# Kernel optimization log

Measured on AMD Instinct MI355X. Metric: run time of the kernel, lower is better.

The kernel has to match this reference:

```python
import jax, jax.numpy as jnp
import numpy as np

T, B, DIN, DLAT = 512, 128, 256, 512

def setup_inputs() -> dict:
    key = jax.random.key(0)
    k1, k2, k3, k4, k5 = jax.random.split(key, 5)
    s_i = 1.0 / np.sqrt(DIN)
    s_h = 1.0 / np.sqrt(DLAT)
    return {
        "X": jax.random.normal(k1, (T, B, DIN), dtype=jnp.float32),
        "h": jnp.zeros((B, DLAT), dtype=jnp.float32),
        "Wi": jax.random.uniform(k2, (DLAT, DIN), jnp.float32, -s_i, s_i),
        "bi": jax.random.uniform(k3, (DLAT,), jnp.float32, -s_i, s_i),
        "Wh": jax.random.uniform(k4, (DLAT, DLAT), jnp.float32, -s_h, s_h),
        "bh": jax.random.uniform(k5, (DLAT,), jnp.float32, -s_h, s_h),
    }

def reference(X, h, Wi, bi, Wh, bh):
    # Precompute input projection for all timesteps at once: [T,B,DLAT]
    Xi = jnp.einsum('tbd,ld->tbl', X, Wi) + bi + bh
    def step(h_prev, xi_t):
        h_t = jnp.tanh(xi_t + h_prev @ Wh.T)  # [B, DLAT]
        return h_t, h_t
    _, H = jax.lax.scan(step, h, Xi)
    return H  # [T, B, DLAT]
```

## Files before the change

kernel.cpp:

```cpp
#include <hip/hip_runtime.h>

#define T_STEPS 512
#define BATCH   128
#define DIN     256
#define DLAT    512

typedef __bf16 bf16x8 __attribute__((ext_vector_type(8)));
typedef float  f32x4  __attribute__((ext_vector_type(4)));
typedef int    i32x4  __attribute__((ext_vector_type(4)));
typedef unsigned long long u64;

__device__ __forceinline__ unsigned int f2bf2(float a, float b) {
  unsigned int ua = __float_as_uint(a);
  unsigned int ub = __float_as_uint(b);
  ua = (ua + 0x7FFFu + ((ua >> 16) & 1u)) >> 16;
  ub = (ub + 0x7FFFu + ((ub >> 16) & 1u)) >> 16;
  return ua | (ub << 16);
}

__device__ __forceinline__ uint4 pack8(float4 f0, float4 f1) {
  uint4 r;
  r.x = f2bf2(f0.x, f0.y);
  r.y = f2bf2(f0.z, f0.w);
  r.z = f2bf2(f1.x, f1.y);
  r.w = f2bf2(f1.z, f1.w);
  return r;
}

extern "C" __global__ __launch_bounds__(256) void pk_wh(
    const float* __restrict__ Wh, unsigned int* __restrict__ out) {
  int idx = blockIdx.x * 256 + threadIdx.x;
  const float* src = Wh + (long)idx * 8;
  float4 f0 = *(const float4*)src;
  float4 f1 = *(const float4*)(src + 4);
  uint4 v = pack8(f0, f1);
  *(uint4*)(out + (long)idx * 4) = v;
}

extern "C" __global__ __launch_bounds__(256) void xi_gemm(
    const float* __restrict__ X, const float* __restrict__ Wi,
    const float* __restrict__ bi, const float* __restrict__ bh,
    float* __restrict__ XiOut) {
  extern __shared__ char smem[];
  char*  sX    = smem;
  char*  sW    = smem + 65536;
  float* sBias = (float*)(smem + 131072);

  const int tid = threadIdx.x;
  const long m0 = (long)blockIdx.x * 128;
  const int  n0 = blockIdx.y * 128;

  #pragma unroll
  for (int c = 0; c < 16; ++c) {
    int id = c * 256 + tid;
    int r  = id >> 5;
    int kc = (id & 31) << 3;
    const float* sx = X + (m0 + r) * DIN + kc;
    float4 a0 = *(const float4*)sx;
    float4 a1 = *(const float4*)(sx + 4);
    int ax = ((r << 9) + (kc << 1)) ^ ((r & 7) << 4);
    *(uint4*)(sX + ax) = pack8(a0, a1);
    const float* sw = Wi + (n0 + r) * DIN + kc;
    float4 b0 = *(const float4*)sw;
    float4 b1 = *(const float4*)(sw + 4);
    *(uint4*)(sW + ax) = pack8(b0, b1);
  }
  if (tid < 128) sBias[tid] = bi[n0 + tid] + bh[n0 + tid];
  __syncthreads();

  const int w = tid >> 6, lane = tid & 63;
  const int wm = (w >> 1) * 64, wn = (w & 1) * 64;
  const int lm = lane & 15, lq = lane >> 4;

  f32x4 acc[4][4];
  #pragma unroll
  for (int nt = 0; nt < 4; ++nt) {
    float bv = sBias[wn + nt * 16 + lm];
    #pragma unroll
    for (int mt = 0; mt < 4; ++mt) acc[mt][nt] = f32x4{bv, bv, bv, bv};
  }

  #pragma unroll
  for (int k0 = 0; k0 < 8; ++k0) {
    int kb = (k0 << 6) + (lq << 4);
    bf16x8 af[4], bfr[4];
    #pragma unroll
    for (int mt = 0; mt < 4; ++mt) {
      int row = wm + mt * 16 + lm;
      int ax = ((row << 9) + kb) ^ ((row & 7) << 4);
      af[mt] = __builtin_bit_cast(bf16x8, *(uint4*)(sX + ax));
    }
    #pragma unroll
    for (int nt = 0; nt < 4; ++nt) {
      int row = wn + nt * 16 + lm;
      int ax = ((row << 9) + kb) ^ ((row & 7) << 4);
      bfr[nt] = __builtin_bit_cast(bf16x8, *(uint4*)(sW + ax));
    }
    #pragma unroll
    for (int mt = 0; mt < 4; ++mt)
      #pragma unroll
      for (int nt = 0; nt < 4; ++nt)
        acc[mt][nt] = __builtin_amdgcn_mfma_f32_16x16x32_bf16(af[mt], bfr[nt], acc[mt][nt], 0, 0, 0);
  }

  #pragma unroll
  for (int mt = 0; mt < 4; ++mt) {
    #pragma unroll
    for (int e = 0; e < 4; ++e) {
      long m = m0 + wm + mt * 16 + (lq << 2) + e;
      float* dst = XiOut + m * DLAT + n0 + wn + lm;
      #pragma unroll
      for (int nt = 0; nt < 4; ++nt)
        dst[nt * 16] = acc[mt][nt][e];
    }
  }
}

extern "C" __global__ __launch_bounds__(512, 2) void rnn_scan(
    const float* __restrict__ h0, const unsigned short* __restrict__ WhP,
    float* __restrict__ HO, u64* __restrict__ hx,
    unsigned int* __restrict__ flags) {
  __shared__ uint4 sH4[1024];
  char* sH = (char*)sH4;

  const int tid = threadIdx.x;
  const int w = tid >> 6, lane = tid & 63;
  const int lm = lane & 15, lq = lane >> 4;
  const int g  = blockIdx.x & 7;
  const int q  = blockIdx.x >> 3;
  const int r0 = g << 4;
  const int nt = (q << 7) + (w << 4);

  i32x4 wreg[16];
  {
    const unsigned short* base = WhP + (nt + lm) * DLAT + (lq << 3);
    #pragma unroll
    for (int kq = 0; kq < 16; ++kq)
      wreg[kq] = *(const i32x4*)(base + kq * 32);
    #pragma unroll
    for (int kq = 0; kq < 16; ++kq)
      asm("" : "+v"(wreg[kq]));
  }

  #pragma unroll
  for (int c = 0; c < 2; ++c) {
    int id = c * 512 + tid;
    int m = id >> 6, kc = (id & 63) << 3;
    const float* src = h0 + (r0 + m) * DLAT + kc;
    float4 f0 = *(const float4*)src;
    float4 f1 = *(const float4*)(src + 4);
    int ax = ((m << 10) + (kc << 1)) ^ ((m & 7) << 4);
    *(uint4*)(sH + ax) = pack8(f0, f1);
  }
  __syncthreads();

  const int mask  = (lm & 7) << 4;
  const int hbase = (lm << 10) + (lq << 4);
  const int ncol  = nt + (lq << 2);
  unsigned int* fgrp = flags + (g << 11);
  const int sq = (q + 1 + lane) & 3;

  float4 xi = *(const float4*)(HO + (long)(r0 + lm) * DLAT + ncol);

  for (int t = 0; t < T_STEPS; ++t) {
    f32x4 a0 = f32x4{0.f, 0.f, 0.f, 0.f};
    f32x4 a1 = f32x4{0.f, 0.f, 0.f, 0.f};
    f32x4 a2 = f32x4{0.f, 0.f, 0.f, 0.f};
    f32x4 a3 = f32x4{0.f, 0.f, 0.f, 0.f};
    #pragma unroll
    for (int kq = 0; kq < 16; kq += 4) {
      bf16x8 hb0 = __builtin_bit_cast(bf16x8, *(uint4*)(sH + ((hbase + kq * 64) ^ mask)));
      bf16x8 hb1 = __builtin_bit_cast(bf16x8, *(uint4*)(sH + ((hbase + (kq + 1) * 64) ^ mask)));
      bf16x8 hb2 = __builtin_bit_cast(bf16x8, *(uint4*)(sH + ((hbase + (kq + 2) * 64) ^ mask)));
      bf16x8 hb3 = __builtin_bit_cast(bf16x8, *(uint4*)(sH + ((hbase + (kq + 3) * 64) ^ mask)));
      a0 = __builtin_amdgcn_mfma_f32_16x16x32_bf16(
          __builtin_bit_cast(bf16x8, wreg[kq]), hb0, a0, 0, 0, 0);
      a1 = __builtin_amdgcn_mfma_f32_16x16x32_bf16(
          __builtin_bit_cast(bf16x8, wreg[kq + 1]), hb1, a1, 0, 0, 0);
      a2 = __builtin_amdgcn_mfma_f32_16x16x32_bf16(
          __builtin_bit_cast(bf16x8, wreg[kq + 2]), hb2, a2, 0, 0, 0);
      a3 = __builtin_amdgcn_mfma_f32_16x16x32_bf16(
          __builtin_bit_cast(bf16x8, wreg[kq + 3]), hb3, a3, 0, 0, 0);
    }

    float hv[4];
    #pragma unroll
    for (int e = 0; e < 4; ++e) {
      float z = (a0[e] + a1[e]) + (a2[e] + a3[e]) + ((float*)&xi)[e];
      float ex = __expf(2.0f * z);
      hv[e] = 1.0f - 2.0f / (ex + 1.0f);
    }

    if (t + 1 < T_STEPS) {
      u64* hxg = hx + ((long)(t & 1) << 14) + ((long)g << 11);
      u64 v = ((u64)f2bf2(hv[2], hv[3]) << 32) | (u64)f2bf2(hv[0], hv[1]);

      __hip_atomic_store(&hxg[(lm << 7) + (ncol >> 2)], v,
                         __ATOMIC_RELAXED, __HIP_MEMORY_SCOPE_AGENT);
      asm volatile("s_waitcnt vmcnt(0)" ::: "memory");
      __syncthreads();

      if (tid == 0)
        __hip_atomic_store(&fgrp[(q << 9) + t], 1u,
                           __ATOMIC_RELAXED, __HIP_MEMORY_SCOPE_AGENT);

      {
        int ax = ((lm << 10) + (ncol << 1)) ^ mask;
        *(u64*)(sH + ax) = v;
        float4 o; o.x = hv[0]; o.y = hv[1]; o.z = hv[2]; o.w = hv[3];
        *(float4*)(HO + ((long)t * BATCH + r0 + lm) * DLAT + ncol) = o;
        xi = *(const float4*)(HO + ((long)(t + 1) * BATCH + r0 + lm) * DLAT + ncol);
      }

      for (;;) {
        unsigned int fv = (lane < 3)
            ? __hip_atomic_load(&fgrp[(sq << 9) + t], __ATOMIC_RELAXED, __HIP_MEMORY_SCOPE_AGENT)
            : 1u;
        if (!__any(fv == 0u)) break;
        __builtin_amdgcn_s_sleep(1);
      }
      asm volatile("" ::: "memory");

      {
        int m = tid >> 5, j = tid & 31;
        #pragma unroll
        for (int s = 1; s < 4; ++s) {
          int qq = (q + s) & 3;
          int idx = (m << 7) + (qq << 5) + j;
          u64 hvv = __hip_atomic_load(&hxg[idx],
                                      __ATOMIC_RELAXED, __HIP_MEMORY_SCOPE_AGENT);
          int ax = ((m << 10) + (((qq << 5) + j) << 3)) ^ ((m & 7) << 4);
          *(u64*)(sH + ax) = hvv;
        }
      }

      __syncthreads();
    } else {
      float4 o; o.x = hv[0]; o.y = hv[1]; o.z = hv[2]; o.w = hv[3];
      *(float4*)(HO + ((long)t * BATCH + r0 + lm) * DLAT + ncol) = o;
    }
  }
}

extern "C" void kernel_launch(void* const* d_in, const int* in_sizes, int n_in,
                              void* d_out, int out_size, void* d_ws, size_t ws_size,
                              hipStream_t stream) {
  const float* X  = (const float*)d_in[0];
  const float* h0 = (const float*)d_in[1];
  const float* Wi = (const float*)d_in[2];
  const float* bi = (const float*)d_in[3];
  const float* Wh = (const float*)d_in[4];
  const float* bh = (const float*)d_in[5];
  float* out = (float*)d_out;

  unsigned int* whp   = (unsigned int*)d_ws;
  u64*          hx    = (u64*)((char*)d_ws + 524288);
  unsigned int* flags = (unsigned int*)((char*)d_ws + 786432);

  hipMemsetAsync(flags, 0, 65536, stream);

  hipFuncSetAttribute((const void*)xi_gemm, hipFuncAttributeMaxDynamicSharedMemorySize, 131584);

  pk_wh<<<128, 256, 0, stream>>>(Wh, whp);
  xi_gemm<<<dim3(512, 4), 256, 131584, stream>>>(X, Wi, bi, bh, out);
  rnn_scan<<<32, 512, 0, stream>>>(h0, (const unsigned short*)whp, out, hx, flags);
}
```

Before: 1.306 ms.

## Load recurrent h fragments directly from global exchange buffer, drop LDS staging

The scan kernel no longer copies the exchanged hidden state into shared memory each step. Each lane now reads its MFMA B-operand fragments straight from the double-buffered global exchange array. A new pk_h0 kernel seeds buffer 0 with the bf16-packed initial state. This removes the per-step LDS write, the LDS re-read and one block-wide barrier from the serial critical path. In exchange, every wave issues 32 global loads per step and re-reads the full 16x512 state, so L2 traffic rises sharply and L2 latency moves onto the MFMA input path.

```diff
diff --git a/kernel.cpp b/kernel.cpp
--- a/kernel.cpp
+++ b/kernel.cpp
@@ -9,6 +9,7 @@
 typedef float  f32x4  __attribute__((ext_vector_type(4)));
 typedef int    i32x4  __attribute__((ext_vector_type(4)));
 typedef unsigned long long u64;
+typedef unsigned long long u64x2 __attribute__((ext_vector_type(2)));
 
 __device__ __forceinline__ unsigned int f2bf2(float a, float b) {
   unsigned int ua = __float_as_uint(a);
@@ -35,6 +36,16 @@
   float4 f1 = *(const float4*)(src + 4);
   uint4 v = pack8(f0, f1);
   *(uint4*)(out + (long)idx * 4) = v;
+}
+
+extern "C" __global__ __launch_bounds__(256) void pk_h0(
+    const float* __restrict__ h0, u64* __restrict__ hx) {
+  int idx = blockIdx.x * 256 + threadIdx.x;
+  int r = idx >> 7, j = idx & 127;
+  int g = r >> 4, m = r & 15;
+  float4 f = *(const float4*)(h0 + (long)r * DLAT + j * 4);
+  u64 v = ((u64)f2bf2(f.z, f.w) << 32) | (u64)f2bf2(f.x, f.y);
+  hx[((long)g << 11) + (m << 7) + j] = v;
 }
 
 extern "C" __global__ __launch_bounds__(256) void xi_gemm(
@@ -117,12 +128,8 @@
 }
 
 extern "C" __global__ __launch_bounds__(512, 2) void rnn_scan(
-    const float* __restrict__ h0, const unsigned short* __restrict__ WhP,
-    float* __restrict__ HO, u64* __restrict__ hx,
-    unsigned int* __restrict__ flags) {
-  __shared__ uint4 sH4[1024];
-  char* sH = (char*)sH4;
-
+    const unsigned short* __restrict__ WhP, float* __restrict__ HO,
+    u64* __restrict__ hx, unsigned int* __restrict__ flags) {
   const int tid = threadIdx.x;
   const int w = tid >> 6, lane = tid & 63;
   const int lm = lane & 15, lq = lane >> 4;
@@ -142,45 +149,43 @@
       asm("" : "+v"(wreg[kq]));
   }
 
-  #pragma unroll
-  for (int c = 0; c < 2; ++c) {
-    int id = c * 512 + tid;
-    int m = id >> 6, kc = (id & 63) << 3;
-    const float* src = h0 + (r0 + m) * DLAT + kc;
-    float4 f0 = *(const float4*)src;
-    float4 f1 = *(const float4*)(src + 4);
-    int ax = ((m << 10) + (kc << 1)) ^ ((m & 7) << 4);
-    *(uint4*)(sH + ax) = pack8(f0, f1);
-  }
-  __syncthreads();
-
-  const int mask  = (lm & 7) << 4;
-  const int hbase = (lm << 10) + (lq << 4);
-  const int ncol  = nt + (lq << 2);
+  const int ncol = nt + (lq << 2);
   unsigned int* fgrp = flags + (g << 11);
   const int sq = (q + 1 + lane) & 3;
+  u64* hgrp = hx + ((long)g << 11);
+  const int fb  = (lm << 7) + (lq << 1);
+  const int pub = (lm << 7) + (ncol >> 2);
 
   float4 xi = *(const float4*)(HO + (long)(r0 + lm) * DLAT + ncol);
 
   for (int t = 0; t < T_STEPS; ++t) {
+    const u64* hs = hgrp + ((long)(t & 1) << 14);
+
+    u64 fA[16], fB[16];
+    #pragma unroll
+    for (int kq = 0; kq < 16; ++kq) {
+      fA[kq] = __hip_atomic_load(&hs[fb + kq * 8],     __ATOMIC_RELAXED, __HIP_MEMORY_SCOPE_AGENT);
+      fB[kq] = __hip_atomic_load(&hs[fb + kq * 8 + 1], __ATOMIC_RELAXED, __HIP_MEMORY_SCOPE_AGENT);
+    }
+
     f32x4 a0 = f32x4{0.f, 0.f, 0.f, 0.f};
     f32x4 a1 = f32x4{0.f, 0.f, 0.f, 0.f};
     f32x4 a2 = f32x4{0.f, 0.f, 0.f, 0.f};
     f32x4 a3 = f32x4{0.f, 0.f, 0.f, 0.f};
     #pragma unroll
     for (int kq = 0; kq < 16; kq += 4) {
-      bf16x8 hb0 = __builtin_bit_cast(bf16x8, *(uint4*)(sH + ((hbase + kq * 64) ^ mask)));
-      bf16x8 hb1 = __builtin_bit_cast(bf16x8, *(uint4*)(sH + ((hbase + (kq + 1) * 64) ^ mask)));
-      bf16x8 hb2 = __builtin_bit_cast(bf16x8, *(uint4*)(sH + ((hbase + (kq + 2) * 64) ^ mask)));
-      bf16x8 hb3 = __builtin_bit_cast(bf16x8, *(uint4*)(sH + ((hbase + (kq + 3) * 64) ^ mask)));
+      u64x2 p0 = u64x2{fA[kq],     fB[kq]};
+      u64x2 p1 = u64x2{fA[kq + 1], fB[kq + 1]};
+      u64x2 p2 = u64x2{fA[kq + 2], fB[kq + 2]};
+      u64x2 p3 = u64x2{fA[kq + 3], fB[kq + 3]};
       a0 = __builtin_amdgcn_mfma_f32_16x16x32_bf16(
-          __builtin_bit_cast(bf16x8, wreg[kq]), hb0, a0, 0, 0, 0);
+          __builtin_bit_cast(bf16x8, wreg[kq]),     __builtin_bit_cast(bf16x8, p0), a0, 0, 0, 0);
       a1 = __builtin_amdgcn_mfma_f32_16x16x32_bf16(
-          __builtin_bit_cast(bf16x8, wreg[kq + 1]), hb1, a1, 0, 0, 0);
+          __builtin_bit_cast(bf16x8, wreg[kq + 1]), __builtin_bit_cast(bf16x8, p1), a1, 0, 0, 0);
       a2 = __builtin_amdgcn_mfma_f32_16x16x32_bf16(
-          __builtin_bit_cast(bf16x8, wreg[kq + 2]), hb2, a2, 0, 0, 0);
+          __builtin_bit_cast(bf16x8, wreg[kq + 2]), __builtin_bit_cast(bf16x8, p2), a2, 0, 0, 0);
       a3 = __builtin_amdgcn_mfma_f32_16x16x32_bf16(
-          __builtin_bit_cast(bf16x8, wreg[kq + 3]), hb3, a3, 0, 0, 0);
+          __builtin_bit_cast(bf16x8, wreg[kq + 3]), __builtin_bit_cast(bf16x8, p3), a3, 0, 0, 0);
     }
 
     float hv[4];
@@ -192,10 +197,8 @@
     }
 
     if (t + 1 < T_STEPS) {
-      u64* hxg = hx + ((long)(t & 1) << 14) + ((long)g << 11);
       u64 v = ((u64)f2bf2(hv[2], hv[3]) << 32) | (u64)f2bf2(hv[0], hv[1]);
-
-      __hip_atomic_store(&hxg[(lm << 7) + (ncol >> 2)], v,
+      __hip_atomic_store(&hgrp[((long)((t + 1) & 1) << 14) + pub], v,
                          __ATOMIC_RELAXED, __HIP_MEMORY_SCOPE_AGENT);
       asm volatile("s_waitcnt vmcnt(0)" ::: "memory");
       __syncthreads();
@@ -205,8 +208,6 @@
                            __ATOMIC_RELAXED, __HIP_MEMORY_SCOPE_AGENT);
 
       {
-        int ax = ((lm << 10) + (ncol << 1)) ^ mask;
-        *(u64*)(sH + ax) = v;
         float4 o; o.x = hv[0]; o.y = hv[1]; o.z = hv[2]; o.w = hv[3];
         *(float4*)(HO + ((long)t * BATCH + r0 + lm) * DLAT + ncol) = o;
         xi = *(const float4*)(HO + ((long)(t + 1) * BATCH + r0 + lm) * DLAT + ncol);
@@ -220,21 +221,6 @@
         __builtin_amdgcn_s_sleep(1);
       }
       asm volatile("" ::: "memory");
-
-      {
-        int m = tid >> 5, j = tid & 31;
-        #pragma unroll
-        for (int s = 1; s < 4; ++s) {
-          int qq = (q + s) & 3;
-          int idx = (m << 7) + (qq << 5) + j;
-          u64 hvv = __hip_atomic_load(&hxg[idx],
-                                      __ATOMIC_RELAXED, __HIP_MEMORY_SCOPE_AGENT);
-          int ax = ((m << 10) + (((qq << 5) + j) << 3)) ^ ((m & 7) << 4);
-          *(u64*)(sH + ax) = hvv;
-        }
-      }
-
-      __syncthreads();
     } else {
       float4 o; o.x = hv[0]; o.y = hv[1]; o.z = hv[2]; o.w = hv[3];
       *(float4*)(HO + ((long)t * BATCH + r0 + lm) * DLAT + ncol) = o;
@@ -262,6 +248,7 @@
   hipFuncSetAttribute((const void*)xi_gemm, hipFuncAttributeMaxDynamicSharedMemorySize, 131584);
 
   pk_wh<<<128, 256, 0, stream>>>(Wh, whp);
+  pk_h0<<<64, 256, 0, stream>>>(h0, hx);
   xi_gemm<<<dim3(512, 4), 256, 131584, stream>>>(X, Wi, bi, bh, out);
-  rnn_scan<<<32, 512, 0, stream>>>(h0, (const unsigned short*)whp, out, hx, flags);
-}
+  rnn_scan<<<32, 512, 0, stream>>>((const unsigned short*)whp, out, hx, flags);
+}
```

New measurement: 4.325 ms. +231.0%, slower.

## Replace flag-based cross-block sync with tagged data words and double-buffered LDS

Applied to the files above, without the earlier changes.

Each published bf16 hidden value now carries the step index in its upper 16 bits, so consumer blocks poll the data itself instead of waiting for a separate flag store after a vmcnt wait and block barrier. This removes one __syncthreads, the store-to-flag round trip and the sleep in the spin loop. The shared-memory hidden state is double-buffered so the next step's buffer can be filled without a barrier before the MFMA reads of the current one. In exchange, the exchange traffic doubles because each bf16 value occupies 32 bits, and polling becomes more aggressive without s_sleep.

```diff
diff --git a/kernel.cpp b/kernel.cpp
--- a/kernel.cpp
+++ b/kernel.cpp
@@ -118,10 +118,9 @@
 
 extern "C" __global__ __launch_bounds__(512, 2) void rnn_scan(
     const float* __restrict__ h0, const unsigned short* __restrict__ WhP,
-    float* __restrict__ HO, u64* __restrict__ hx,
-    unsigned int* __restrict__ flags) {
-  __shared__ uint4 sH4[1024];
-  char* sH = (char*)sH4;
+    float* __restrict__ HO, u64* __restrict__ hx) {
+  __shared__ uint4 sHbuf[2048];
+  char* sB = (char*)sHbuf;
 
   const int tid = threadIdx.x;
   const int w = tid >> 6, lane = tid & 63;
@@ -150,29 +149,38 @@
     float4 f0 = *(const float4*)src;
     float4 f1 = *(const float4*)(src + 4);
     int ax = ((m << 10) + (kc << 1)) ^ ((m & 7) << 4);
-    *(uint4*)(sH + ax) = pack8(f0, f1);
+    *(uint4*)(sB + ax) = pack8(f0, f1);
   }
   __syncthreads();
 
   const int mask  = (lm & 7) << 4;
   const int hbase = (lm << 10) + (lq << 4);
   const int ncol  = nt + (lq << 2);
-  unsigned int* fgrp = flags + (g << 11);
-  const int sq = (q + 1 + lane) & 3;
+  u64* hgrp = hx + ((long)g << 12);
+  const int pubi = (lm << 8) + (ncol >> 1);
+  const int rm = tid >> 5, rj = tid & 31;
+  const int q1 = (q + 1) & 3, q2 = (q + 2) & 3, q3 = (q + 3) & 3;
+  const int i1 = (rm << 8) + (q1 << 6) + (rj << 1);
+  const int i2 = (rm << 8) + (q2 << 6) + (rj << 1);
+  const int i3 = (rm << 8) + (q3 << 6) + (rj << 1);
+  const u64 tagmask = 0xFFFF0000FFFF0000ull;
 
   float4 xi = *(const float4*)(HO + (long)(r0 + lm) * DLAT + ncol);
 
   for (int t = 0; t < T_STEPS; ++t) {
+    char* cur = sB + ((t & 1) << 14);
+    char* nxt = sB + (((t + 1) & 1) << 14);
+
     f32x4 a0 = f32x4{0.f, 0.f, 0.f, 0.f};
     f32x4 a1 = f32x4{0.f, 0.f, 0.f, 0.f};
     f32x4 a2 = f32x4{0.f, 0.f, 0.f, 0.f};
     f32x4 a3 = f32x4{0.f, 0.f, 0.f, 0.f};
     #pragma unroll
     for (int kq = 0; kq < 16; kq += 4) {
-      bf16x8 hb0 = __builtin_bit_cast(bf16x8, *(uint4*)(sH + ((hbase + kq * 64) ^ mask)));
-      bf16x8 hb1 = __builtin_bit_cast(bf16x8, *(uint4*)(sH + ((hbase + (kq + 1) * 64) ^ mask)));
-      bf16x8 hb2 = __builtin_bit_cast(bf16x8, *(uint4*)(sH + ((hbase + (kq + 2) * 64) ^ mask)));
-      bf16x8 hb3 = __builtin_bit_cast(bf16x8, *(uint4*)(sH + ((hbase + (kq + 3) * 64) ^ mask)));
+      bf16x8 hb0 = __builtin_bit_cast(bf16x8, *(uint4*)(cur + ((hbase + kq * 64) ^ mask)));
+      bf16x8 hb1 = __builtin_bit_cast(bf16x8, *(uint4*)(cur + ((hbase + (kq + 1) * 64) ^ mask)));
+      bf16x8 hb2 = __builtin_bit_cast(bf16x8, *(uint4*)(cur + ((hbase + (kq + 2) * 64) ^ mask)));
+      bf16x8 hb3 = __builtin_bit_cast(bf16x8, *(uint4*)(cur + ((hbase + (kq + 3) * 64) ^ mask)));
       a0 = __builtin_amdgcn_mfma_f32_16x16x32_bf16(
           __builtin_bit_cast(bf16x8, wreg[kq]), hb0, a0, 0, 0, 0);
       a1 = __builtin_amdgcn_mfma_f32_16x16x32_bf16(
@@ -191,47 +199,60 @@
       hv[e] = 1.0f - 2.0f / (ex + 1.0f);
     }
 
+    unsigned int pr01 = f2bf2(hv[0], hv[1]);
+    unsigned int pr23 = f2bf2(hv[2], hv[3]);
+
     if (t + 1 < T_STEPS) {
-      u64* hxg = hx + ((long)(t & 1) << 14) + ((long)g << 11);
-      u64 v = ((u64)f2bf2(hv[2], hv[3]) << 32) | (u64)f2bf2(hv[0], hv[1]);
-
-      __hip_atomic_store(&hxg[(lm << 7) + (ncol >> 2)], v,
-                         __ATOMIC_RELAXED, __HIP_MEMORY_SCOPE_AGENT);
-      asm volatile("s_waitcnt vmcnt(0)" ::: "memory");
-      __syncthreads();
-
-      if (tid == 0)
-        __hip_atomic_store(&fgrp[(q << 9) + t], 1u,
-                           __ATOMIC_RELAXED, __HIP_MEMORY_SCOPE_AGENT);
+      u64* ps = hgrp + ((long)((t + 1) & 1) << 15);
+      {
+        unsigned int tg = (unsigned int)(t + 1) << 16;
+        u64 p0 = (u64)(tg | (pr01 & 0xFFFFu)) | ((u64)(tg | (pr01 >> 16)) << 32);
+        u64 p1 = (u64)(tg | (pr23 & 0xFFFFu)) | ((u64)(tg | (pr23 >> 16)) << 32);
+        __hip_atomic_store(&ps[pubi],     p0, __ATOMIC_RELAXED, __HIP_MEMORY_SCOPE_AGENT);
+        __hip_atomic_store(&ps[pubi + 1], p1, __ATOMIC_RELAXED, __HIP_MEMORY_SCOPE_AGENT);
+      }
 
       {
         int ax = ((lm << 10) + (ncol << 1)) ^ mask;
-        *(u64*)(sH + ax) = v;
+        *(u64*)(nxt + ax) = (u64)pr01 | ((u64)pr23 << 32);
+      }
+      {
         float4 o; o.x = hv[0]; o.y = hv[1]; o.z = hv[2]; o.w = hv[3];
         *(float4*)(HO + ((long)t * BATCH + r0 + lm) * DLAT + ncol) = o;
         xi = *(const float4*)(HO + ((long)(t + 1) * BATCH + r0 + lm) * DLAT + ncol);
       }
 
-      for (;;) {
-        unsigned int fv = (lane < 3)
-            ? __hip_atomic_load(&fgrp[(sq << 9) + t], __ATOMIC_RELAXED, __HIP_MEMORY_SCOPE_AGENT)
-            : 1u;
-        if (!__any(fv == 0u)) break;
-        __builtin_amdgcn_s_sleep(1);
-      }
-      asm volatile("" ::: "memory");
-
-      {
-        int m = tid >> 5, j = tid & 31;
-        #pragma unroll
-        for (int s = 1; s < 4; ++s) {
-          int qq = (q + s) & 3;
-          int idx = (m << 7) + (qq << 5) + j;
-          u64 hvv = __hip_atomic_load(&hxg[idx],
-                                      __ATOMIC_RELAXED, __HIP_MEMORY_SCOPE_AGENT);
-          int ax = ((m << 10) + (((qq << 5) + j) << 3)) ^ ((m & 7) << 4);
-          *(u64*)(sH + ax) = hvv;
+      u64 d1a, d1b, d2a, d2b, d3a, d3b;
+      {
+        const u64 tagpat = ((u64)(unsigned int)(t + 1) << 48) |
+                           ((u64)(unsigned int)(t + 1) << 16);
+        for (;;) {
+          d1a = __hip_atomic_load(&ps[i1],     __ATOMIC_RELAXED, __HIP_MEMORY_SCOPE_AGENT);
+          d1b = __hip_atomic_load(&ps[i1 + 1], __ATOMIC_RELAXED, __HIP_MEMORY_SCOPE_AGENT);
+          d2a = __hip_atomic_load(&ps[i2],     __ATOMIC_RELAXED, __HIP_MEMORY_SCOPE_AGENT);
+          d2b = __hip_atomic_load(&ps[i2 + 1], __ATOMIC_RELAXED, __HIP_MEMORY_SCOPE_AGENT);
+          d3a = __hip_atomic_load(&ps[i3],     __ATOMIC_RELAXED, __HIP_MEMORY_SCOPE_AGENT);
+          d3b = __hip_atomic_load(&ps[i3 + 1], __ATOMIC_RELAXED, __HIP_MEMORY_SCOPE_AGENT);
+          bool ok = ((d1a & tagmask) == tagpat) & ((d1b & tagmask) == tagpat) &
+                    ((d2a & tagmask) == tagpat) & ((d2b & tagmask) == tagpat) &
+                    ((d3a & tagmask) == tagpat) & ((d3b & tagmask) == tagpat);
+          if (!__any(!ok)) break;
         }
+      }
+
+      {
+        u64 v1 = (d1a & 0xFFFFull) | (((d1a >> 32) & 0xFFFFull) << 16) |
+                 ((d1b & 0xFFFFull) << 32) | (((d1b >> 32) & 0xFFFFull) << 48);
+        u64 v2 = (d2a & 0xFFFFull) | (((d2a >> 32) & 0xFFFFull) << 16) |
+                 ((d2b & 0xFFFFull) << 32) | (((d2b >> 32) & 0xFFFFull) << 48);
+        u64 v3 = (d3a & 0xFFFFull) | (((d3a >> 32) & 0xFFFFull) << 16) |
+                 ((d3b & 0xFFFFull) << 32) | (((d3b >> 32) & 0xFFFFull) << 48);
+        int ax1 = ((rm << 10) + (q1 << 8) + (rj << 3)) ^ ((rm & 7) << 4);
+        int ax2 = ((rm << 10) + (q2 << 8) + (rj << 3)) ^ ((rm & 7) << 4);
+        int ax3 = ((rm << 10) + (q3 << 8) + (rj << 3)) ^ ((rm & 7) << 4);
+        *(u64*)(nxt + ax1) = v1;
+        *(u64*)(nxt + ax2) = v2;
+        *(u64*)(nxt + ax3) = v3;
       }
 
       __syncthreads();
@@ -253,15 +274,14 @@
   const float* bh = (const float*)d_in[5];
   float* out = (float*)d_out;
 
-  unsigned int* whp   = (unsigned int*)d_ws;
-  u64*          hx    = (u64*)((char*)d_ws + 524288);
-  unsigned int* flags = (unsigned int*)((char*)d_ws + 786432);
-
-  hipMemsetAsync(flags, 0, 65536, stream);
+  unsigned int* whp = (unsigned int*)d_ws;
+  u64*          hx  = (u64*)((char*)d_ws + 524288);
+
+  hipMemsetAsync(hx, 0, 524288, stream);
 
   hipFuncSetAttribute((const void*)xi_gemm, hipFuncAttributeMaxDynamicSharedMemorySize, 131584);
 
   pk_wh<<<128, 256, 0, stream>>>(Wh, whp);
   xi_gemm<<<dim3(512, 4), 256, 131584, stream>>>(X, Wi, bi, bh, out);
-  rnn_scan<<<32, 512, 0, stream>>>(h0, (const unsigned short*)whp, out, hx, flags);
-}
+  rnn_scan<<<32, 512, 0, stream>>>(h0, (const unsigned short*)whp, out, hx);
+}
```

Measured after the change: 1.697 ms. 29.9% more time.

## Split each batch group across two blocks instead of four in RNN scan

Applied to the files above, without the earlier changes.

Halves the blocks per batch group from four to two, so each block holds 32 output columns per wave and keeps twice as many Wh fragments in registers. Cross-block exchange per step then needs only one partner flag and half the remote hidden-state data. The poll loop now speculatively loads the partner data while spinning and drops the sleep. In exchange each block does twice the MFMA work per step and register pressure rises, and the speculative loads rely on the relaxed ordering between the data and flag loads.

```diff
diff --git a/kernel.cpp b/kernel.cpp
--- a/kernel.cpp
+++ b/kernel.cpp
@@ -127,20 +127,23 @@
   const int w = tid >> 6, lane = tid & 63;
   const int lm = lane & 15, lq = lane >> 4;
   const int g  = blockIdx.x & 7;
-  const int q  = blockIdx.x >> 3;
+  const int p  = blockIdx.x >> 3;
   const int r0 = g << 4;
-  const int nt = (q << 7) + (w << 4);
-
-  i32x4 wreg[16];
-  {
-    const unsigned short* base = WhP + (nt + lm) * DLAT + (lq << 3);
+  const int nt = (p << 8) + (w << 5);
+
+  i32x4 wreg[2][16];
+  #pragma unroll
+  for (int t0 = 0; t0 < 2; ++t0) {
+    const unsigned short* base = WhP + (nt + t0 * 16 + lm) * DLAT + (lq << 3);
     #pragma unroll
     for (int kq = 0; kq < 16; ++kq)
-      wreg[kq] = *(const i32x4*)(base + kq * 32);
+      wreg[t0][kq] = *(const i32x4*)(base + kq * 32);
+  }
+  #pragma unroll
+  for (int t0 = 0; t0 < 2; ++t0)
     #pragma unroll
     for (int kq = 0; kq < 16; ++kq)
-      asm("" : "+v"(wreg[kq]));
-  }
+      asm("" : "+v"(wreg[t0][kq]));
 
   #pragma unroll
   for (int c = 0; c < 2; ++c) {
@@ -158,86 +161,106 @@
   const int hbase = (lm << 10) + (lq << 4);
   const int ncol  = nt + (lq << 2);
   unsigned int* fgrp = flags + (g << 11);
-  const int sq = (q + 1 + lane) & 3;
-
-  float4 xi = *(const float4*)(HO + (long)(r0 + lm) * DLAT + ncol);
+  const int sp = p ^ 1;
+  const int rm = tid >> 5, rj = tid & 31;
+  const int i1 = (rm << 7) + (sp << 6) + rj;
+  const int i2 = i1 + 32;
+
+  float4 xi0, xi1;
+  {
+    const float* xr = HO + (long)(r0 + lm) * DLAT + ncol;
+    xi0 = *(const float4*)xr;
+    xi1 = *(const float4*)(xr + 16);
+  }
 
   for (int t = 0; t < T_STEPS; ++t) {
-    f32x4 a0 = f32x4{0.f, 0.f, 0.f, 0.f};
-    f32x4 a1 = f32x4{0.f, 0.f, 0.f, 0.f};
-    f32x4 a2 = f32x4{0.f, 0.f, 0.f, 0.f};
-    f32x4 a3 = f32x4{0.f, 0.f, 0.f, 0.f};
-    #pragma unroll
-    for (int kq = 0; kq < 16; kq += 4) {
+    f32x4 a00 = f32x4{0.f, 0.f, 0.f, 0.f};
+    f32x4 a01 = f32x4{0.f, 0.f, 0.f, 0.f};
+    f32x4 a10 = f32x4{0.f, 0.f, 0.f, 0.f};
+    f32x4 a11 = f32x4{0.f, 0.f, 0.f, 0.f};
+    #pragma unroll
+    for (int kq = 0; kq < 16; kq += 2) {
       bf16x8 hb0 = __builtin_bit_cast(bf16x8, *(uint4*)(sH + ((hbase + kq * 64) ^ mask)));
       bf16x8 hb1 = __builtin_bit_cast(bf16x8, *(uint4*)(sH + ((hbase + (kq + 1) * 64) ^ mask)));
-      bf16x8 hb2 = __builtin_bit_cast(bf16x8, *(uint4*)(sH + ((hbase + (kq + 2) * 64) ^ mask)));
-      bf16x8 hb3 = __builtin_bit_cast(bf16x8, *(uint4*)(sH + ((hbase + (kq + 3) * 64) ^ mask)));
-      a0 = __builtin_amdgcn_mfma_f32_16x16x32_bf16(
-          __builtin_bit_cast(bf16x8, wreg[kq]), hb0, a0, 0, 0, 0);
-      a1 = __builtin_amdgcn_mfma_f32_16x16x32_bf16(
-          __builtin_bit_cast(bf16x8, wreg[kq + 1]), hb1, a1, 0, 0, 0);
-      a2 = __builtin_amdgcn_mfma_f32_16x16x32_bf16(
-          __builtin_bit_cast(bf16x8, wreg[kq + 2]), hb2, a2, 0, 0, 0);
-      a3 = __builtin_amdgcn_mfma_f32_16x16x32_bf16(
-          __builtin_bit_cast(bf16x8, wreg[kq + 3]), hb3, a3, 0, 0, 0);
-    }
-
-    float hv[4];
+      a00 = __builtin_amdgcn_mfma_f32_16x16x32_bf16(
+          __builtin_bit_cast(bf16x8, wreg[0][kq]), hb0, a00, 0, 0, 0);
+      a10 = __builtin_amdgcn_mfma_f32_16x16x32_bf16(
+          __builtin_bit_cast(bf16x8, wreg[1][kq]), hb0, a10, 0, 0, 0);
+      a01 = __builtin_amdgcn_mfma_f32_16x16x32_bf16(
+          __builtin_bit_cast(bf16x8, wreg[0][kq + 1]), hb1, a01, 0, 0, 0);
+      a11 = __builtin_amdgcn_mfma_f32_16x16x32_bf16(
+          __builtin_bit_cast(bf16x8, wreg[1][kq + 1]), hb1, a11, 0, 0, 0);
+    }
+
+    float hv0[4], hv1[4];
     #pragma unroll
     for (int e = 0; e < 4; ++e) {
-      float z = (a0[e] + a1[e]) + (a2[e] + a3[e]) + ((float*)&xi)[e];
-      float ex = __expf(2.0f * z);
-      hv[e] = 1.0f - 2.0f / (ex + 1.0f);
-    }
+      float z0 = (a00[e] + a01[e]) + ((float*)&xi0)[e];
+      float z1 = (a10[e] + a11[e]) + ((float*)&xi1)[e];
+      float e0 = __expf(2.0f * z0);
+      float e1 = __expf(2.0f * z1);
+      hv0[e] = 1.0f - 2.0f / (e0 + 1.0f);
+      hv1[e] = 1.0f - 2.0f / (e1 + 1.0f);
+    }
+
+    u64 v0 = (u64)f2bf2(hv0[0], hv0[1]) | ((u64)f2bf2(hv0[2], hv0[3]) << 32);
+    u64 v1 = (u64)f2bf2(hv1[0], hv1[1]) | ((u64)f2bf2(hv1[2], hv1[3]) << 32);
 
     if (t + 1 < T_STEPS) {
       u64* hxg = hx + ((long)(t & 1) << 14) + ((long)g << 11);
-      u64 v = ((u64)f2bf2(hv[2], hv[3]) << 32) | (u64)f2bf2(hv[0], hv[1]);
-
-      __hip_atomic_store(&hxg[(lm << 7) + (ncol >> 2)], v,
-                         __ATOMIC_RELAXED, __HIP_MEMORY_SCOPE_AGENT);
+      const int pubi = (lm << 7) + (ncol >> 2);
+
+      __hip_atomic_store(&hxg[pubi],     v0, __ATOMIC_RELAXED, __HIP_MEMORY_SCOPE_AGENT);
+      __hip_atomic_store(&hxg[pubi + 4], v1, __ATOMIC_RELAXED, __HIP_MEMORY_SCOPE_AGENT);
       asm volatile("s_waitcnt vmcnt(0)" ::: "memory");
       __syncthreads();
 
       if (tid == 0)
-        __hip_atomic_store(&fgrp[(q << 9) + t], 1u,
+        __hip_atomic_store(&fgrp[(p << 9) + t], 1u,
                            __ATOMIC_RELAXED, __HIP_MEMORY_SCOPE_AGENT);
 
       {
-        int ax = ((lm << 10) + (ncol << 1)) ^ mask;
-        *(u64*)(sH + ax) = v;
-        float4 o; o.x = hv[0]; o.y = hv[1]; o.z = hv[2]; o.w = hv[3];
-        *(float4*)(HO + ((long)t * BATCH + r0 + lm) * DLAT + ncol) = o;
-        xi = *(const float4*)(HO + ((long)(t + 1) * BATCH + r0 + lm) * DLAT + ncol);
+        int ax0 = ((lm << 10) + (ncol << 1)) ^ mask;
+        int ax1 = ((lm << 10) + ((ncol + 16) << 1)) ^ mask;
+        *(u64*)(sH + ax0) = v0;
+        *(u64*)(sH + ax1) = v1;
+        float* orow = HO + ((long)t * BATCH + r0 + lm) * DLAT + ncol;
+        float4 o0; o0.x = hv0[0]; o0.y = hv0[1]; o0.z = hv0[2]; o0.w = hv0[3];
+        float4 o1; o1.x = hv1[0]; o1.y = hv1[1]; o1.z = hv1[2]; o1.w = hv1[3];
+        *(float4*)orow = o0;
+        *(float4*)(orow + 16) = o1;
+        const float* xr = HO + ((long)(t + 1) * BATCH + r0 + lm) * DLAT + ncol;
+        xi0 = *(const float4*)xr;
+        xi1 = *(const float4*)(xr + 16);
       }
 
+      u64 d1, d2;
       for (;;) {
-        unsigned int fv = (lane < 3)
-            ? __hip_atomic_load(&fgrp[(sq << 9) + t], __ATOMIC_RELAXED, __HIP_MEMORY_SCOPE_AGENT)
+        d1 = __hip_atomic_load(&hxg[i1], __ATOMIC_RELAXED, __HIP_MEMORY_SCOPE_AGENT);
+        d2 = __hip_atomic_load(&hxg[i2], __ATOMIC_RELAXED, __HIP_MEMORY_SCOPE_AGENT);
+        unsigned int fv = (lane == 0)
+            ? __hip_atomic_load(&fgrp[(sp << 9) + t], __ATOMIC_RELAXED, __HIP_MEMORY_SCOPE_AGENT)
             : 1u;
         if (!__any(fv == 0u)) break;
-        __builtin_amdgcn_s_sleep(1);
       }
       asm volatile("" ::: "memory");
 
       {
-        int m = tid >> 5, j = tid & 31;
-        #pragma unroll
-        for (int s = 1; s < 4; ++s) {
-          int qq = (q + s) & 3;
-          int idx = (m << 7) + (qq << 5) + j;
-          u64 hvv = __hip_atomic_load(&hxg[idx],
-                                      __ATOMIC_RELAXED, __HIP_MEMORY_SCOPE_AGENT);
-          int ax = ((m << 10) + (((qq << 5) + j) << 3)) ^ ((m & 7) << 4);
-          *(u64*)(sH + ax) = hvv;
-        }
+        int c1 = (sp << 6) + rj;
+        int c2 = c1 + 32;
+        int ax1 = ((rm << 10) + (c1 << 3)) ^ ((rm & 7) << 4);
+        int ax2 = ((rm << 10) + (c2 << 3)) ^ ((rm & 7) << 4);
+        *(u64*)(sH + ax1) = d1;
+        *(u64*)(sH + ax2) = d2;
       }
 
       __syncthreads();
     } else {
-      float4 o; o.x = hv[0]; o.y = hv[1]; o.z = hv[2]; o.w = hv[3];
-      *(float4*)(HO + ((long)t * BATCH + r0 + lm) * DLAT + ncol) = o;
+      float* orow = HO + ((long)t * BATCH + r0 + lm) * DLAT + ncol;
+      float4 o0; o0.x = hv0[0]; o0.y = hv0[1]; o0.z = hv0[2]; o0.w = hv0[3];
+      float4 o1; o1.x = hv1[0]; o1.y = hv1[1]; o1.z = hv1[2]; o1.w = hv1[3];
+      *(float4*)orow = o0;
+      *(float4*)(orow + 16) = o1;
     }
   }
 }
@@ -263,5 +286,5 @@
 
   pk_wh<<<128, 256, 0, stream>>>(Wh, whp);
   xi_gemm<<<dim3(512, 4), 256, 131584, stream>>>(X, Wi, bi, bh, out);
-  rnn_scan<<<32, 512, 0, stream>>>(h0, (const unsigned short*)whp, out, hx, flags);
-}
+  rnn_scan<<<16, 512, 0, stream>>>(h0, (const unsigned short*)whp, out, hx, flags);
+}
```

After: 1.522 ms. 1.17x slower.
